# Kernel tuning notes

Hardware: AMD Instinct MI355X
Metric: run time of the kernel (lower is better)

Reference implementation:

```python
import jax, jax.numpy as jnp
import numpy as np


def _make_cameras(key, B):
    """Well-conditioned c = [cam2world(16), intrinsics(9)] per batch."""
    k1, k2 = jax.random.split(key)
    # random rotation via Gram-Schmidt on a random 3x3
    A = jax.random.normal(k1, (B, 3, 3), dtype=jnp.float32)
    q0 = A[:, :, 0] / jnp.linalg.norm(A[:, :, 0], axis=-1, keepdims=True)
    v1 = A[:, :, 1] - jnp.sum(A[:, :, 1] * q0, -1, keepdims=True) * q0
    q1 = v1 / jnp.linalg.norm(v1, axis=-1, keepdims=True)
    q2 = jnp.cross(q0, q1)
    R = jnp.stack([q0, q1, q2], axis=-1)                      # [B,3,3]
    t = 2.7 * q2                                              # camera at radius 2.7 along view axis
    cam2world = jnp.zeros((B, 4, 4), jnp.float32)
    cam2world = cam2world.at[:, :3, :3].set(R)
    cam2world = cam2world.at[:, :3, 3].set(t)
    cam2world = cam2world.at[:, 3, 3].set(1.0)
    # EG3D-style normalized intrinsics: fx=fy=4.2647, cx=cy=0.5, sk=0
    intr = jnp.tile(jnp.array([[4.2647, 0.0, 0.5],
                               [0.0, 4.2647, 0.5],
                               [0.0, 0.0, 1.0]], jnp.float32), (B, 1, 1))
    return jnp.concatenate([cam2world.reshape(B, 16), intr.reshape(B, 9)], axis=1)


def setup_inputs() -> dict:
    key = jax.random.key(0)
    kc, kd, kp = jax.random.split(key, 3)
    B, R, M = 8, 64, 4096
    c = _make_cameras(kc, B)
    image_depth = 2.2 + 1.1 * jax.random.uniform(kd, (B, R * R, 1), dtype=jnp.float32)
    pc = 0.3 * jax.random.normal(kp, (B, M, 3), dtype=jnp.float32)
    return {"c": c, "image_depth": image_depth, "pc": pc, "resolution": R}


def _ray_sampler(cam2world, intrinsics, resolution):
    B = cam2world.shape[0]
    N = resolution * resolution
    fx = intrinsics[:, 0, 0][:, None]
    fy = intrinsics[:, 1, 1][:, None]
    cx = intrinsics[:, 0, 2][:, None]
    cy = intrinsics[:, 1, 2][:, None]
    sk = intrinsics[:, 0, 1][:, None]
    r = (jnp.arange(resolution, dtype=jnp.float32) + 0.5) / resolution
    gi, gj = jnp.meshgrid(r, r, indexing='ij')                # row, col
    x_cam = jnp.broadcast_to(gj.reshape(-1), (B, N))          # uv.flip(0): x is col coord
    y_cam = jnp.broadcast_to(gi.reshape(-1), (B, N))
    z_cam = jnp.ones((B, N), jnp.float32)
    x_lift = (x_cam - cx + cy * sk / fy - sk * y_cam / fy) / fx * z_cam
    y_lift = (y_cam - cy) / fy * z_cam
    cam_rel = jnp.stack([x_lift, y_lift, z_cam, jnp.ones_like(z_cam)], axis=-1)  # [B,N,4]
    world = jnp.einsum('bij,bnj->bni', cam2world, cam_rel)[..., :3]
    origins = cam2world[:, :3, 3]                              # [B,3]
    dirs = world - origins[:, None, :]
    dirs = dirs / jnp.linalg.norm(dirs, axis=-1, keepdims=True)
    ray_origins = jnp.broadcast_to(origins[:, None, :], dirs.shape)
    return ray_origins, dirs


def _chamfer(x, y):
    # squared-distance NN both directions; GEMM-form pairwise distances
    x2 = jnp.sum(x * x, axis=-1)                               # [B,N]
    y2 = jnp.sum(y * y, axis=-1)                               # [B,M]
    xy = jnp.einsum('bnd,bmd->bnm', x, y)                      # [B,N,M]
    d = x2[:, :, None] + y2[:, None, :] - 2.0 * xy
    return jnp.min(d, axis=2), jnp.min(d, axis=1)              # dist1 [B,N], dist2 [B,M]


def reference(c, image_depth, pc, resolution):
    B = c.shape[0]
    pc = pc[..., :3]
    depth = image_depth.reshape(B, -1, 1)
    cam2world = c[:, :16].reshape(-1, 4, 4)
    intr = c[:, 16:25].reshape(-1, 3, 3)
    ro, rd = _ray_sampler(cam2world, intr, resolution)
    pred_pos = depth * rd + ro                                  # [B,N,3]
    d0, d1 = _chamfer(pred_pos, pc)
    K = min(pred_pos.shape[1], pc.shape[1]) // 2
    d0s = jnp.sort(d0, axis=1)[:, :K]
    d1s = d0s  # NOTE: faithful to original code (loss_1_sorted is assigned from loss_0_sorted)
    loss0 = jnp.mean(d0s, axis=1)
    loss1 = jnp.mean(d1s, axis=1)
    return (loss0 + loss1).reshape(B, 1)
```

## Files before the change

kernel.cpp:

```cpp
#include <hip/hip_runtime.h>
#include <math.h>

#define FLT_BIG 3.0e38f
#define HIST_BINS 16384
#define CNT_STRIDE 64

__global__ __launch_bounds__(256, 2) void chamfer_fused_kernel(
    const float* __restrict__ cparam,
    const float* __restrict__ depth,
    const float* __restrict__ pc,
    float* __restrict__ d0,
    unsigned int* __restrict__ cnt,
    float* __restrict__ out,
    int N, int M, int R, int K)
{
    const int b   = blockIdx.y;
    const int tid = threadIdx.x;

    extern __shared__ float4 s4[];

    const float* pcb = pc + (size_t)b * M * 3;
    for (int idx = tid; idx < M; idx += 256) {
        float x = pcb[idx * 3 + 0];
        float y = pcb[idx * 3 + 1];
        float z = pcb[idx * 3 + 2];
        s4[idx] = make_float4(x, y, z, 0.5f * (x * x + y * y + z * z));
    }
    __syncthreads();

    const float* cb = cparam + (size_t)b * 25;
    const float fx = cb[16], sk = cb[17], cx = cb[18];
    const float fy = cb[20], cy = cb[21];

    const int chunk = tid & 31;
    const int grp   = tid >> 5;
    const int nbase = blockIdx.x * 64 + grp * 8;

    const int i0 = nbase / R;
    const int j0 = nbase - i0 * R;
    const float y_cam = (i0 + 0.5f) / (float)R;
    const float y_lift = (y_cam - cy) / fy;
    const float base_x = (-cx + cy * sk / fy - sk * y_cam / fy);

    float px[8], py[8], pz[8], e[8];
    #pragma unroll
    for (int r = 0; r < 8; r++) {
        const float x_cam = (j0 + r + 0.5f) / (float)R;
        const float x_lift = (x_cam + base_x) / fx;
        const float dxw = cb[0] * x_lift + cb[1] * y_lift + cb[2];
        const float dyw = cb[4] * x_lift + cb[5] * y_lift + cb[6];
        const float dzw = cb[8] * x_lift + cb[9] * y_lift + cb[10];
        const float inv = 1.0f / sqrtf(dxw * dxw + dyw * dyw + dzw * dzw);
        const float dep = depth[(size_t)b * N + nbase + r];
        px[r] = cb[3]  + dep * dxw * inv;
        py[r] = cb[7]  + dep * dyw * inv;
        pz[r] = cb[11] + dep * dzw * inv;
        e[r]  = FLT_BIG;
    }

    const int Mc = M >> 5;
    for (int m = 0; m < Mc; m += 8) {
        float4 q[8];
        #pragma unroll
        for (int mm = 0; mm < 8; mm++)
            q[mm] = s4[((m + mm) << 5) + chunk];
        #pragma unroll
        for (int mm = 0; mm < 8; mm++) {
            #pragma unroll
            for (int r = 0; r < 8; r++) {
                float t = fmaf(-px[r], q[mm].x, q[mm].w);
                t = fmaf(-py[r], q[mm].y, t);
                t = fmaf(-pz[r], q[mm].z, t);
                e[r] = fminf(e[r], t);
            }
        }
    }

    #pragma unroll
    for (int r = 0; r < 8; r++) {
        float v = e[r];
        v = fminf(v, __shfl_xor(v, 1));
        v = fminf(v, __shfl_xor(v, 2));
        v = fminf(v, __shfl_xor(v, 4));
        v = fminf(v, __shfl_xor(v, 8));
        v = fminf(v, __shfl_xor(v, 16));
        e[r] = v;
    }
    if (chunk == 0) {
        #pragma unroll
        for (int r = 0; r < 8; r++) {
            const float pn = px[r] * px[r] + py[r] * py[r] + pz[r] * pz[r];
            d0[(size_t)b * N + nbase + r] = fmaxf(2.0f * e[r] + pn, 0.0f);
        }
    }

    __shared__ unsigned int is_last;
    __syncthreads();
    if (tid == 0) {
        __threadfence();
        unsigned int old = atomicAdd(&cnt[b * CNT_STRIDE], 1u);
        is_last = (old == gridDim.x - 1) ? 1u : 0u;
    }
    __syncthreads();
    if (!is_last) return;
    __threadfence();

    unsigned int* hist = (unsigned int*)s4;
    __shared__ unsigned int spart[256];
    __shared__ unsigned int s_selbin, s_krem;
    __shared__ unsigned int subcnt[32];
    __shared__ float        subsum[32];
    __shared__ float        s_below;

    for (int t2 = tid; t2 < HIST_BINS; t2 += 256) hist[t2] = 0u;
    if (tid < 32) { subcnt[tid] = 0u; subsum[tid] = 0.0f; }
    if (tid == 0) s_below = 0.0f;
    __syncthreads();

    unsigned int key[16];
    #pragma unroll
    for (int t2 = 0; t2 < 16; t2++)
        key[t2] = __float_as_uint(d0[(size_t)b * N + t2 * 256 + tid]);
    #pragma unroll
    for (int t2 = 0; t2 < 16; t2++)
        atomicAdd(&hist[key[t2] >> 18], 1u);
    __syncthreads();

    unsigned int psum = 0u;
    #pragma unroll 8
    for (int i2 = 0; i2 < 64; i2++)
        psum += hist[(tid << 6) + ((i2 + tid) & 63)];
    spart[tid] = psum;
    __syncthreads();

    unsigned int cbef = 0u;
    for (int i2 = 0; i2 < tid; i2++) cbef += spart[i2];
    if (cbef < (unsigned int)K && (unsigned int)K <= cbef + psum) {
        unsigned int k2 = (unsigned int)K - cbef;
        unsigned int sel = 0u;
        for (int i2 = 0; i2 < 64; i2++) {
            unsigned int h = hist[(tid << 6) + i2];
            if (k2 <= h) { sel = (tid << 6) + i2; break; }
            k2 -= h;
        }
        s_selbin = sel;
        s_krem   = k2;
    }
    __syncthreads();

    const unsigned int selbin = s_selbin;
    float sumb = 0.0f;
    #pragma unroll
    for (int t2 = 0; t2 < 16; t2++) {
        const unsigned int bin = key[t2] >> 18;
        const float v = __uint_as_float(key[t2]);
        if (bin < selbin) sumb += v;
        if (bin == selbin) {
            const unsigned int sub = (key[t2] >> 13) & 31u;
            atomicAdd(&subcnt[sub], 1u);
            atomicAdd(&subsum[sub], v);
        }
    }
    atomicAdd(&s_below, sumb);
    __syncthreads();

    if (tid == 0) {
        unsigned int k2 = s_krem;
        float s = s_below;
        for (int i2 = 0; i2 < 32; i2++) {
            unsigned int h = subcnt[i2];
            if (k2 <= h) {
                s += (h ? (subsum[i2] * ((float)k2 / (float)h)) : 0.0f);
                break;
            }
            s += subsum[i2];
            k2 -= h;
        }
        out[b] = 2.0f * s / (float)K;
    }
}

extern "C" void kernel_launch(void* const* d_in, const int* in_sizes, int n_in,
                              void* d_out, int out_size, void* d_ws, size_t ws_size,
                              hipStream_t stream)
{
    const float* c   = (const float*)d_in[0];
    const float* dep = (const float*)d_in[1];
    const float* pc  = (const float*)d_in[2];
    float* out = (float*)d_out;

    const int B = in_sizes[0] / 25;
    const int N = in_sizes[1] / B;
    const int M = in_sizes[2] / (3 * B);
    int R = 1; while (R * R < N) R++;

    float* d0 = (float*)d_ws;
    unsigned int* cnt = (unsigned int*)(d0 + (size_t)B * N);

    hipMemsetAsync(cnt, 0, (size_t)B * CNT_STRIDE * sizeof(unsigned int), stream);

    const int K = ((N < M) ? N : M) / 2;
    dim3 grid(N / 64, B);
    size_t lds = (size_t)M * sizeof(float4);
    if (lds < HIST_BINS * sizeof(unsigned int)) lds = HIST_BINS * sizeof(unsigned int);
    hipLaunchKernelGGL(chamfer_fused_kernel, grid, dim3(256), lds, stream,
                       c, dep, pc, d0, cnt, out, N, M, R, K);
}
```

Before: 96.14 us.

## Split fused chamfer kernel into separate min and select-mean kernels

Replaces the last-block-done atomic counter scheme with two kernel launches: one computes per-ray nearest-neighbour distances, the second does the histogram-based top-K mean per batch. This drops the memset, per-block atomics and threadfences from the hot kernel, and lets the LDS size be set to exactly M float4 rather than the histogram maximum. The cost is an extra kernel launch and a global-memory round trip for d0 between kernels.

```diff
diff --git a/kernel.cpp b/kernel.cpp
--- a/kernel.cpp
+++ b/kernel.cpp
@@ -3,16 +3,13 @@
 
 #define FLT_BIG 3.0e38f
 #define HIST_BINS 16384
-#define CNT_STRIDE 64
-
-__global__ __launch_bounds__(256, 2) void chamfer_fused_kernel(
+
+__global__ __launch_bounds__(256, 2) void chamfer_min_kernel(
     const float* __restrict__ cparam,
     const float* __restrict__ depth,
     const float* __restrict__ pc,
     float* __restrict__ d0,
-    unsigned int* __restrict__ cnt,
-    float* __restrict__ out,
-    int N, int M, int R, int K)
+    int N, int M, int R)
 {
     const int b   = blockIdx.y;
     const int tid = threadIdx.x;
@@ -93,19 +90,17 @@
             d0[(size_t)b * N + nbase + r] = fmaxf(2.0f * e[r] + pn, 0.0f);
         }
     }
-
-    __shared__ unsigned int is_last;
-    __syncthreads();
-    if (tid == 0) {
-        __threadfence();
-        unsigned int old = atomicAdd(&cnt[b * CNT_STRIDE], 1u);
-        is_last = (old == gridDim.x - 1) ? 1u : 0u;
-    }
-    __syncthreads();
-    if (!is_last) return;
-    __threadfence();
-
-    unsigned int* hist = (unsigned int*)s4;
+}
+
+__global__ __launch_bounds__(256, 1) void select_mean_kernel(
+    const float* __restrict__ d0,
+    float* __restrict__ out,
+    int N, int K)
+{
+    const int b   = blockIdx.x;
+    const int tid = threadIdx.x;
+
+    extern __shared__ unsigned int hist[];
     __shared__ unsigned int spart[256];
     __shared__ unsigned int s_selbin, s_krem;
     __shared__ unsigned int subcnt[32];
@@ -195,14 +190,14 @@
     int R = 1; while (R * R < N) R++;
 
     float* d0 = (float*)d_ws;
-    unsigned int* cnt = (unsigned int*)(d0 + (size_t)B * N);
-
-    hipMemsetAsync(cnt, 0, (size_t)B * CNT_STRIDE * sizeof(unsigned int), stream);
+
+    dim3 gridA(N / 64, B);
+    size_t ldsA = (size_t)M * sizeof(float4);
+    hipLaunchKernelGGL(chamfer_min_kernel, gridA, dim3(256), ldsA, stream,
+                       c, dep, pc, d0, N, M, R);
 
     const int K = ((N < M) ? N : M) / 2;
-    dim3 grid(N / 64, B);
-    size_t lds = (size_t)M * sizeof(float4);
-    if (lds < HIST_BINS * sizeof(unsigned int)) lds = HIST_BINS * sizeof(unsigned int);
-    hipLaunchKernelGGL(chamfer_fused_kernel, grid, dim3(256), lds, stream,
-                       c, dep, pc, d0, cnt, out, N, M, R, K);
+    size_t ldsB = (size_t)HIST_BINS * sizeof(unsigned int);
+    hipLaunchKernelGGL(select_mean_kernel, dim3(B), dim3(256), ldsB, stream,
+                       d0, out, N, K);
 }
```

After: 88.11 us. 8.3% less time.
